# Kernel optimization log

Hardware: AMD Instinct MI355X
Metric: run time of the kernel (lower is better)

Reference implementation:

```python
import jax, jax.numpy as jnp
import numpy as np

N = 3072
R = 16
B = 16


def setup_inputs() -> dict:
    key = jax.random.key(0)
    k1, k2, k3, k4, k5 = jax.random.split(key, 5)
    z1 = jax.random.normal(k1, (N, R), dtype=jnp.float32)
    z2 = jax.random.normal(k2, (N, R), dtype=jnp.float32)
    seg_matrix = jax.random.randint(k3, (N, N), 0, 2).astype(jnp.float32)
    cls_label = jax.random.randint(k4, (N,), 0, 30).astype(jnp.int64)
    batch = jnp.sort(jax.random.randint(k5, (N,), 0, B)).astype(jnp.int64)
    return {"z1": z1, "z2": z2, "seg_matrix": seg_matrix,
            "cls_label": cls_label, "batch": batch}


def reference(z1, z2, seg_matrix, cls_label, batch):
    n, r = z1.shape
    # seg_matrix += eye(N): self-pairs never have seg == 0
    seg = seg_matrix + jnp.eye(n, dtype=seg_matrix.dtype)
    # nodes with class labels 24/25/26 are excluded
    node_mask = (cls_label != 24) & (cls_label != 25) & (cls_label != 26)
    # pair (i, j) is written iff both nodes valid, same graph, and seg[i,j] == 0.
    # (the per-batch meshgrid/nonzero loop == same-batch pair condition)
    pair = (node_mask[:, None] & node_mask[None, :]
            & (batch[:, None] == batch[None, :])
            & (seg == 0.0))                              # [N, N]
    # default value: one-hot on relation 0 (concat of ones and zeros)
    default = jax.nn.one_hot(0, r, dtype=z1.dtype)        # [R]
    prod = z1[:, None, :] * z2[None, :, :]                # [N, N, R]
    return jnp.where(pair[:, :, None], prod, default)
```

## Files before the change

kernel.cpp:

```cpp
#include <hip/hip_runtime.h>
#include <cstddef>

#define NN 3072
#define RR 16
#define UNROLL 8

typedef float f32x4 __attribute__((ext_vector_type(4)));

__global__ void frd_key_kernel(const int* __restrict__ cls,
                               const int* __restrict__ batch,
                               int* __restrict__ key) {
    int i = blockIdx.x * blockDim.x + threadIdx.x;
    if (i < NN) {
        int c = cls[i];
        bool valid = (c != 24) && (c != 25) && (c != 26);
        key[i] = valid ? batch[i] : -1;
    }
}

__global__ __launch_bounds__(256)
void frd_main_kernel(const float* __restrict__ z1,
                     const float* __restrict__ z2,
                     const float* __restrict__ seg,
                     const int* __restrict__ key,
                     float* __restrict__ out) {
    const int base = blockIdx.x * (256 * UNROLL) + threadIdx.x;
    const float d0 = ((threadIdx.x & 3) == 0) ? 1.0f : 0.0f;

#pragma unroll
    for (int k = 0; k < UNROLL; ++k) {
        const int idx = base + k * 256;
        const int pair = idx >> 2;
        const int q = idx & 3;
        const int i = pair / NN;
        const int j = pair - i * NN;

        const float s = __builtin_nontemporal_load(seg + pair);
        const int ki = key[i];
        const int kj = key[j];
        const float seg_eff = s + ((i == j) ? 1.0f : 0.0f);
        const bool is_pair = (ki == kj) && (ki >= 0) && (seg_eff == 0.0f);

        const float4 a = *reinterpret_cast<const float4*>(z1 + i * RR + q * 4);
        const float4 b = *reinterpret_cast<const float4*>(z2 + j * RR + q * 4);

        f32x4 r;
        r.x = is_pair ? a.x * b.x : d0;
        r.y = is_pair ? a.y * b.y : 0.0f;
        r.z = is_pair ? a.z * b.z : 0.0f;
        r.w = is_pair ? a.w * b.w : 0.0f;

        __builtin_nontemporal_store(r, reinterpret_cast<f32x4*>(out + (size_t)idx * 4));
    }
}

extern "C" void kernel_launch(void* const* d_in, const int* in_sizes, int n_in,
                              void* d_out, int out_size, void* d_ws, size_t ws_size,
                              hipStream_t stream) {
    const float* z1  = (const float*)d_in[0];
    const float* z2  = (const float*)d_in[1];
    const float* seg = (const float*)d_in[2];
    const int* cls   = (const int*)d_in[3];
    const int* batch = (const int*)d_in[4];
    float* out = (float*)d_out;
    int* key = (int*)d_ws;

    frd_key_kernel<<<(NN + 255) / 256, 256, 0, stream>>>(cls, batch, key);

    const int total = NN * NN * 4;
    frd_main_kernel<<<total / (256 * UNROLL), 256, 0, stream>>>(z1, z2, seg, key, out);
}
```

Measured before the change: 126.6 us.

## Precompute pair mask into byte buffer and restructure main kernel by row

Adds a pre-pass kernel that evaluates the full pair predicate (class validity, same batch, seg==0 with the diagonal rule) and writes one byte per pair into workspace. The main kernel then gives each block one row i and a 512-column slice, loading z1[i] once per thread and reading only the byte mask instead of the float seg matrix plus the key lookups. This removes the per-element division and indexed key gathers from the write-heavy kernel. In exchange it adds a second full pass over seg, an extra write and read of the byte mask, and a kernel launch. The old path is kept as a fallback when the workspace is too small.

```diff
diff --git a/kernel.cpp b/kernel.cpp
--- a/kernel.cpp
+++ b/kernel.cpp
@@ -6,6 +6,56 @@
 #define UNROLL 8
 
 typedef float f32x4 __attribute__((ext_vector_type(4)));
+
+__global__ __launch_bounds__(256)
+void frd_pred_kernel(const float* __restrict__ seg,
+                     const int* __restrict__ cls,
+                     const int* __restrict__ batch,
+                     unsigned char* __restrict__ pred) {
+    const int pair = blockIdx.x * 256 + threadIdx.x;
+    const int i = pair / NN;
+    const int j = pair - i * NN;
+    const float s = __builtin_nontemporal_load(seg + pair);
+    const int ci = cls[i], cj = cls[j];
+    const bool vi = (ci != 24) && (ci != 25) && (ci != 26);
+    const bool vj = (cj != 24) && (cj != 25) && (cj != 26);
+    const bool pb = batch[i] == batch[j];
+    const float seg_eff = s + ((i == j) ? 1.0f : 0.0f);
+    pred[pair] = (vi && vj && pb && (seg_eff == 0.0f)) ? 1 : 0;
+}
+
+__global__ __launch_bounds__(256)
+void frd_main_kernel(const float* __restrict__ z1,
+                     const float* __restrict__ z2,
+                     const unsigned char* __restrict__ pred,
+                     float* __restrict__ out) {
+    const int bid = blockIdx.x;
+    const int i = bid / 6;
+    const int s6 = bid - i * 6;
+    const int tid = threadIdx.x;
+    const int q = tid & 3;
+    const int pin = tid >> 2;
+    const int j0 = s6 * 512 + pin;
+
+    const float4 a = *reinterpret_cast<const float4*>(z1 + i * RR + q * 4);
+    const float d0 = (q == 0) ? 1.0f : 0.0f;
+    const unsigned char* pp = pred + i * NN + j0;
+    const float* bp = z2 + j0 * RR + q * 4;
+    float* op = out + ((size_t)(i * NN + j0) * RR) + q * 4;
+
+#pragma unroll
+    for (int k = 0; k < UNROLL; ++k) {
+        const unsigned char pv = pp[k * 64];
+        const float4 b = *reinterpret_cast<const float4*>(bp + k * 1024);
+        const bool m = pv != 0;
+        f32x4 r;
+        r.x = m ? a.x * b.x : d0;
+        r.y = m ? a.y * b.y : 0.0f;
+        r.z = m ? a.z * b.z : 0.0f;
+        r.w = m ? a.w * b.w : 0.0f;
+        __builtin_nontemporal_store(r, reinterpret_cast<f32x4*>(op + k * 1024));
+    }
+}
 
 __global__ void frd_key_kernel(const int* __restrict__ cls,
                                const int* __restrict__ batch,
@@ -19,14 +69,13 @@
 }
 
 __global__ __launch_bounds__(256)
-void frd_main_kernel(const float* __restrict__ z1,
-                     const float* __restrict__ z2,
-                     const float* __restrict__ seg,
-                     const int* __restrict__ key,
-                     float* __restrict__ out) {
+void frd_fallback_kernel(const float* __restrict__ z1,
+                         const float* __restrict__ z2,
+                         const float* __restrict__ seg,
+                         const int* __restrict__ key,
+                         float* __restrict__ out) {
     const int base = blockIdx.x * (256 * UNROLL) + threadIdx.x;
     const float d0 = ((threadIdx.x & 3) == 0) ? 1.0f : 0.0f;
-
 #pragma unroll
     for (int k = 0; k < UNROLL; ++k) {
         const int idx = base + k * 256;
@@ -34,22 +83,18 @@
         const int q = idx & 3;
         const int i = pair / NN;
         const int j = pair - i * NN;
-
         const float s = __builtin_nontemporal_load(seg + pair);
         const int ki = key[i];
         const int kj = key[j];
         const float seg_eff = s + ((i == j) ? 1.0f : 0.0f);
         const bool is_pair = (ki == kj) && (ki >= 0) && (seg_eff == 0.0f);
-
         const float4 a = *reinterpret_cast<const float4*>(z1 + i * RR + q * 4);
         const float4 b = *reinterpret_cast<const float4*>(z2 + j * RR + q * 4);
-
         f32x4 r;
         r.x = is_pair ? a.x * b.x : d0;
         r.y = is_pair ? a.y * b.y : 0.0f;
         r.z = is_pair ? a.z * b.z : 0.0f;
         r.w = is_pair ? a.w * b.w : 0.0f;
-
         __builtin_nontemporal_store(r, reinterpret_cast<f32x4*>(out + (size_t)idx * 4));
     }
 }
@@ -63,10 +108,15 @@
     const int* cls   = (const int*)d_in[3];
     const int* batch = (const int*)d_in[4];
     float* out = (float*)d_out;
-    int* key = (int*)d_ws;
 
-    frd_key_kernel<<<(NN + 255) / 256, 256, 0, stream>>>(cls, batch, key);
-
-    const int total = NN * NN * 4;
-    frd_main_kernel<<<total / (256 * UNROLL), 256, 0, stream>>>(z1, z2, seg, key, out);
+    if (ws_size >= (size_t)NN * NN) {
+        unsigned char* pred = (unsigned char*)d_ws;
+        frd_pred_kernel<<<NN * NN / 256, 256, 0, stream>>>(seg, cls, batch, pred);
+        frd_main_kernel<<<NN * 6 / 1 , 256, 0, stream>>>(z1, z2, pred, out);
+    } else {
+        int* key = (int*)d_ws;
+        frd_key_kernel<<<(NN + 255) / 256, 256, 0, stream>>>(cls, batch, key);
+        const int total = NN * NN * 4;
+        frd_fallback_kernel<<<total / (256 * UNROLL), 256, 0, stream>>>(z1, z2, seg, key, out);
+    }
 }
```

Result: slower. 135.5 us (+7.0%).
